# Kernel optimization log

Measured on AMD Instinct MI355X. Metric: run time of the kernel, lower is better.

The kernel has to match this reference:

```python
import jax, jax.numpy as jnp
import numpy as np

H = 512  # hidden_size


def _gru_layer(x, Wi, bi, Wh, bh):
    # x: (B, S, D). Precompute input-to-hidden part for all steps.
    B, S, _ = x.shape
    ip = jnp.einsum('bsd,gd->sbg', x, Wi) + bi  # (S, B, 3H)
    h0 = jnp.zeros((B, H), dtype=x.dtype)

    def step(h, ip_t):
        hp = h @ Wh.T + bh                      # (B, 3H)
        r = jax.nn.sigmoid(ip_t[:, :H] + hp[:, :H])
        z = jax.nn.sigmoid(ip_t[:, H:2*H] + hp[:, H:2*H])
        n = jnp.tanh(ip_t[:, 2*H:] + r * hp[:, 2*H:])
        hy = (1.0 - z) * n + z * h
        return hy, hy

    h_last, ys = jax.lax.scan(step, h0, ip)     # ys: (S, B, H)
    return jnp.transpose(ys, (1, 0, 2)), h_last  # (B, S, H), (B, H)


def setup_inputs() -> dict:
    key = jax.random.key(0)
    ks = jax.random.split(key, 9)
    s = 1.0 / np.sqrt(H)
    d = {
        'x': jax.random.normal(ks[0], (32, 2048, 512), dtype=jnp.float32),
        'Wi0': jax.random.uniform(ks[1], (3*H, 512), jnp.float32, -s, s),
        'bi0': jax.random.uniform(ks[2], (3*H,), jnp.float32, -s, s),
        'Wh0': jax.random.uniform(ks[3], (3*H, H), jnp.float32, -s, s),
        'bh0': jax.random.uniform(ks[4], (3*H,), jnp.float32, -s, s),
        'Wi1': jax.random.uniform(ks[5], (3*H, H), jnp.float32, -s, s),
        'bi1': jax.random.uniform(ks[6], (3*H,), jnp.float32, -s, s),
        'Wh1': jax.random.uniform(ks[7], (3*H, H), jnp.float32, -s, s),
        'bh1': jax.random.uniform(ks[8], (3*H,), jnp.float32, -s, s),
    }
    return d


def reference(x, Wi0, bi0, Wh0, bh0, Wi1, bi1, Wh1, bh1):
    y0, _ = _gru_layer(x, Wi0, bi0, Wh0, bh0)
    y1, h1 = _gru_layer(y0, Wi1, bi1, Wh1, bh1)
    return y1, h1  # outputs (B,S,H), last hidden (B,H)
```

## Files before the change

### kernel.cpp

```cpp
#include <hip/hip_runtime.h>
#include <hip/hip_bf16.h>


typedef __bf16    bf16x8 __attribute__((ext_vector_type(8)));
typedef __bf16    bf16x4 __attribute__((ext_vector_type(4)));
typedef float     f32x4  __attribute__((ext_vector_type(4)));
typedef _Float16  f16x2  __attribute__((ext_vector_type(2)));
typedef _Float16  f16x8  __attribute__((ext_vector_type(8)));

#define S_LEN 2048
#define BATCH 32
#define HID   512
#define G3    1536
#define MROWS (BATCH * S_LEN)
#define NWG   16
#define NFL   64

__device__ inline float sigmoid_f(float x) { return 1.f / (1.f + __expf(-x)); }
__device__ inline float tanh_f(float x) {
  float e = __expf(2.f * x);
  return 1.f - 2.f / (e + 1.f);
}

template <typename IPT>
__device__ inline void store_ip(IPT* p, float v) {
  if constexpr (sizeof(IPT) == 4) *p = v;
  else *p = __builtin_bit_cast(unsigned short, (__bf16)v);
}
template <typename IPT>
__device__ inline float4 load_ip4(const IPT* p) {
  if constexpr (sizeof(IPT) == 4) {
    return *(const float4*)p;
  } else {
    ushort4 u = *(const ushort4*)p;
    float4 r;
    r.x = __uint_as_float((unsigned)u.x << 16);
    r.y = __uint_as_float((unsigned)u.y << 16);
    r.z = __uint_as_float((unsigned)u.z << 16);
    r.w = __uint_as_float((unsigned)u.w << 16);
    return r;
  }
}

__global__ void prep_wib(const float* __restrict__ W, __bf16* __restrict__ o) {
  int i = blockIdx.x * 256 + threadIdx.x;
  o[i] = (__bf16)W[i];
}

__global__ void prep_bfrag(const float* __restrict__ W, unsigned int* __restrict__ out) {
  int idx = blockIdx.x * 256 + threadIdx.x;
  int p    = idx / 24576;
  int r    = idx % 24576;
  int mh   = r / 12288;
  int r2   = r % 12288;
  int frag = r2 / 256;
  int lq   = r2 % 256;
  int l    = lq >> 2, d = lq & 3;
  int g    = frag >> 4, ks = frag & 15;
  int row  = g * 512 + p * 32 + mh * 16 + (l & 15);
  int k    = ks * 32 + (l >> 4) * 8 + 2 * d;
  f16x2 pk = { (_Float16)W[(size_t)row * HID + k],
               (_Float16)W[(size_t)row * HID + k + 1] };
  out[idx] = __builtin_bit_cast(unsigned int, pk);
}

template <typename IPT>
__global__ __launch_bounds__(256) void gemm_ip(
    const float* __restrict__ A, const __bf16* __restrict__ Bw,
    const float* __restrict__ bias, IPT* __restrict__ C) {
  constexpr int K = 512;
  __shared__ __align__(16) __bf16 As[64][72];
  __shared__ __align__(16) __bf16 Bs[64][72];
  const int tid  = threadIdx.x;
  const int bm   = blockIdx.y, bn = blockIdx.x;
  const int lane = tid & 63,  wave = tid >> 6;
  const int wr   = wave >> 1, wc   = wave & 1;
  f32x4 acc[2][2] = {};
  const int r = tid >> 2, q = tid & 3;
  const float*  Arow = A  + (size_t)(bm * 64 + r) * K;
  const __bf16* Brow = Bw + (size_t)(bn * 64 + r) * K;

  for (int k0 = 0; k0 < K; k0 += 64) {
    const float4* as = (const float4*)(Arow + k0);
    #pragma unroll
    for (int i = 0; i < 4; ++i) {
      float4 v = as[q + 4 * i];
      bf16x4 pkt = { (__bf16)v.x, (__bf16)v.y, (__bf16)v.z, (__bf16)v.w };
      *(bf16x4*)&As[r][4 * (q + 4 * i)] = pkt;
    }
    const uint4* bs = (const uint4*)(Brow + k0);
    uint4* bd = (uint4*)&Bs[r][0];
    bd[q]     = bs[q];
    bd[q + 4] = bs[q + 4];
    __syncthreads();

    #pragma unroll
    for (int kk = 0; kk < 64; kk += 32) {
      const int kb = kk + 8 * (lane >> 4);
      bf16x8 a0 = *(const bf16x8*)&As[wr * 32 +      (lane & 15)][kb];
      bf16x8 a1 = *(const bf16x8*)&As[wr * 32 + 16 + (lane & 15)][kb];
      bf16x8 b0 = *(const bf16x8*)&Bs[wc * 32 +      (lane & 15)][kb];
      bf16x8 b1 = *(const bf16x8*)&Bs[wc * 32 + 16 + (lane & 15)][kb];
      acc[0][0] = __builtin_amdgcn_mfma_f32_16x16x32_bf16(a0, b0, acc[0][0], 0, 0, 0);
      acc[0][1] = __builtin_amdgcn_mfma_f32_16x16x32_bf16(a0, b1, acc[0][1], 0, 0, 0);
      acc[1][0] = __builtin_amdgcn_mfma_f32_16x16x32_bf16(a1, b0, acc[1][0], 0, 0, 0);
      acc[1][1] = __builtin_amdgcn_mfma_f32_16x16x32_bf16(a1, b1, acc[1][1], 0, 0, 0);
    }
    __syncthreads();
  }

  const int row0 = bm * 64 + wr * 32 + (lane >> 4) * 4;
  const int col0 = bn * 64 + wc * 32 + (lane & 15);
  #pragma unroll
  for (int fm = 0; fm < 2; ++fm)
    #pragma unroll
    for (int fn = 0; fn < 2; ++fn) {
      int n = col0 + fn * 16;
      float bv = bias[n];
      #pragma unroll
      for (int reg = 0; reg < 4; ++reg) {
        size_t off = (size_t)(row0 + fm * 16 + reg) * G3 + n;
        store_ip<IPT>(C + off, acc[fm][fn][reg] + bv);
      }
    }
}

template <typename IPT>
__global__ __launch_bounds__(256, 1) void gru_fused(
    const IPT* __restrict__ ip0,
    const uint4* __restrict__ bfWh0,
    const float* __restrict__ bh0,
    const uint4* __restrict__ bfWh1,
    const uint4* __restrict__ bfWi1,
    const float* __restrict__ bi1,
    const float* __restrict__ bh1,
    float* __restrict__ y1,
    float* __restrict__ hlast,
    unsigned long long* __restrict__ h1buf,
    unsigned long long* __restrict__ y0h,
    unsigned int* __restrict__ fl0,
    unsigned int* __restrict__ fl1) {
  __shared__ __align__(16) uint4 wiB[6144];
  const int bid = blockIdx.x, tid = threadIdx.x;
  const int lane = tid & 63, wave = tid >> 6;
  const int set = wave & 1, mh = wave >> 1;
  const int jj = lane & 15, hi = lane >> 4;
  const int bb = set * 16 + jj;
  const int bbyte = bb * 1024 + hi * 16;
  const int fidx = (lane & 15) * 4 + set + 2 * ((lane >> 4) & 1);

  if (bid < NWG) {
    const int p = bid;
    const int cc0 = p * 32 + mh * 16 + hi * 4;
    uint4 wf[48];
    {
      const uint4* bsrc = bfWh0 + ((size_t)(p * 2 + mh) * 48) * 64 + lane;
      #pragma unroll
      for (int i = 0; i < 48; ++i) wf[i] = bsrc[i * 64];
      #pragma unroll
      for (int i = 0; i < 48; ++i)
        asm volatile("" : "+v"(wf[i].x), "+v"(wf[i].y), "+v"(wf[i].z), "+v"(wf[i].w));
    }
    const float4 bhr4 = *(const float4*)(bh0 + cc0);
    const float4 bhz4 = *(const float4*)(bh0 + 512 + cc0);
    const float4 bhn4 = *(const float4*)(bh0 + 1024 + cc0);
    float hfq[4] = {0.f, 0.f, 0.f, 0.f};

    for (int t = 0; t < S_LEN; ++t) {
      const IPT* bp = ip0 + ((size_t)bb * S_LEN + t) * G3 + cc0;
      float4 ipr = load_ip4<IPT>(bp);
      float4 ipz = load_ip4<IPT>(bp + 512);
      float4 ipn = load_ip4<IPT>(bp + 1024);
      __builtin_amdgcn_sched_barrier(0);

      f32x4 a0 = {}, a1 = {}, a2 = {};
      if (t > 0) {
        const unsigned int* f = fl0 + (size_t)(t - 1) * NFL;
        while (true) {
          unsigned v = __hip_atomic_load(f + fidx, __ATOMIC_RELAXED,
                                         __HIP_MEMORY_SCOPE_AGENT);
          if (__all(v != 0)) break;
          __builtin_amdgcn_s_sleep(1);
        }
        __builtin_amdgcn_sched_barrier(0);

        const char* hb = (const char*)y0h + (size_t)(t - 1) * 32768 + bbyte;
        uint4 bf[16];
        #pragma unroll
        for (int ks = 0; ks < 16; ++ks)
          asm volatile("global_load_dwordx4 %0, %1, off offset:%2 sc0 sc1"
                       : "=v"(bf[ks]) : "v"(hb), "i"(ks * 64) : "memory");
        asm volatile("s_waitcnt vmcnt(0)" ::: "memory");
        __builtin_amdgcn_sched_barrier(0);

        #pragma unroll
        for (int ks = 0; ks < 16; ++ks) {
          f16x8 hv = __builtin_bit_cast(f16x8, bf[ks]);
          a0 = __builtin_amdgcn_mfma_f32_16x16x32_f16(__builtin_bit_cast(f16x8, wf[ks]),      hv, a0, 0, 0, 0);
          a1 = __builtin_amdgcn_mfma_f32_16x16x32_f16(__builtin_bit_cast(f16x8, wf[16 + ks]), hv, a1, 0, 0, 0);
          a2 = __builtin_amdgcn_mfma_f32_16x16x32_f16(__builtin_bit_cast(f16x8, wf[32 + ks]), hv, a2, 0, 0, 0);
        }
      }

      unsigned short hx[4];
      #pragma unroll
      for (int q = 0; q < 4; ++q) {
        float rr = sigmoid_f(a0[q] + (&bhr4.x)[q] + (&ipr.x)[q]);
        float zz = sigmoid_f(a1[q] + (&bhz4.x)[q] + (&ipz.x)[q]);
        float nn = tanh_f((&ipn.x)[q] + rr * (a2[q] + (&bhn4.x)[q]));
        float hy = (1.f - zz) * nn + zz * hfq[q];
        hfq[q] = hy;
        hx[q] = __builtin_bit_cast(unsigned short, (_Float16)hy);
      }
      const unsigned long long hw =
          (unsigned long long)hx[0] | ((unsigned long long)hx[1] << 16) |
          ((unsigned long long)hx[2] << 32) | ((unsigned long long)hx[3] << 48);
      __hip_atomic_store(y0h + (size_t)t * 4096 + (size_t)bb * 128 + (cc0 >> 2), hw,
                         __ATOMIC_RELAXED, __HIP_MEMORY_SCOPE_AGENT);
      asm volatile("s_waitcnt vmcnt(0)" ::: "memory");
      if (lane == 0)
        __hip_atomic_store(fl0 + (size_t)t * NFL + p * 4 + wave, 1u,
                           __ATOMIC_RELAXED, __HIP_MEMORY_SCOPE_AGENT);
    }
  } else {
    const int p = bid - NWG;
    const int cc0 = p * 32 + mh * 16 + hi * 4;
    uint4 wf[48];
    {
      const uint4* bsrc = bfWh1 + ((size_t)(p * 2 + mh) * 48) * 64 + lane;
      #pragma unroll
      for (int i = 0; i < 48; ++i) wf[i] = bsrc[i * 64];
      #pragma unroll
      for (int i = 0; i < 48; ++i)
        asm volatile("" : "+v"(wf[i].x), "+v"(wf[i].y), "+v"(wf[i].z), "+v"(wf[i].w));
    }
    {
      const uint4* src = bfWi1 + (size_t)p * 6144;
      for (int i = tid; i < 6144; i += 256) wiB[i] = src[i];
    }
    const float4 bir4 = *(const float4*)(bi1 + cc0);
    const float4 biz4 = *(const float4*)(bi1 + 512 + cc0);
    const float4 bin4 = *(const float4*)(bi1 + 1024 + cc0);
    const float4 bhr4 = *(const float4*)(bh1 + cc0);
    const float4 bhz4 = *(const float4*)(bh1 + 512 + cc0);
    const float4 bhn4 = *(const float4*)(bh1 + 1024 + cc0);
    float hfq[4] = {0.f, 0.f, 0.f, 0.f};
    const int wb = mh * 3072 + lane;
    __syncthreads();

    f32x4 i0 = {}, i1 = {}, i2 = {};
    {
      const unsigned int* f = fl0;
      while (true) {
        unsigned v = __hip_atomic_load(f + fidx, __ATOMIC_RELAXED,
                                       __HIP_MEMORY_SCOPE_AGENT);
        if (__all(v != 0)) break;
        __builtin_amdgcn_s_sleep(16);
      }
      __builtin_amdgcn_sched_barrier(0);
      uint4 ay[16];
      const char* yb = (const char*)y0h + bbyte;
      #pragma unroll
      for (int ks = 0; ks < 16; ++ks)
        asm volatile("global_load_dwordx4 %0, %1, off offset:%2 sc0 sc1"
                     : "=v"(ay[ks]) : "v"(yb), "i"(ks * 64) : "memory");
      asm volatile("s_waitcnt vmcnt(0)" ::: "memory");
      __builtin_amdgcn_sched_barrier(0);
      #pragma unroll
      for (int ks = 0; ks < 16; ++ks) {
        f16x8 yv = __builtin_bit_cast(f16x8, ay[ks]);
        i0 = __builtin_amdgcn_mfma_f32_16x16x32_f16(__builtin_bit_cast(f16x8, wiB[wb + ks * 64]),        yv, i0, 0, 0, 0);
        i1 = __builtin_amdgcn_mfma_f32_16x16x32_f16(__builtin_bit_cast(f16x8, wiB[wb + (16 + ks) * 64]), yv, i1, 0, 0, 0);
        i2 = __builtin_amdgcn_mfma_f32_16x16x32_f16(__builtin_bit_cast(f16x8, wiB[wb + (32 + ks) * 64]), yv, i2, 0, 0, 0);
      }
    }

    for (int t = 0; t < S_LEN; ++t) {
      if (t > 0) {
        const unsigned int* f = fl1 + (size_t)(t - 1) * NFL;
        while (true) {
          unsigned v = __hip_atomic_load(f + fidx, __ATOMIC_RELAXED,
                                         __HIP_MEMORY_SCOPE_AGENT);
          if (__all(v != 0)) break;
          __builtin_amdgcn_s_sleep(16);
        }
      }
      __builtin_amdgcn_sched_barrier(0);

      uint4 ah[16];
      {
        const char* hb = (const char*)h1buf + (t & 1) * 32768 + bbyte;
        #pragma unroll
        for (int ks = 0; ks < 16; ++ks)
          asm volatile("global_load_dwordx4 %0, %1, off offset:%2 sc0 sc1"
                       : "=v"(ah[ks]) : "v"(hb), "i"(ks * 64) : "memory");
        asm volatile("s_waitcnt vmcnt(0)" ::: "memory");
      }
      __builtin_amdgcn_sched_barrier(0);

      f32x4 c0 = {}, c1 = {}, c2 = {};
      #pragma unroll
      for (int ks = 0; ks < 16; ++ks) {
        f16x8 hv = __builtin_bit_cast(f16x8, ah[ks]);
        c0 = __builtin_amdgcn_mfma_f32_16x16x32_f16(__builtin_bit_cast(f16x8, wf[ks]),      hv, c0, 0, 0, 0);
        c1 = __builtin_amdgcn_mfma_f32_16x16x32_f16(__builtin_bit_cast(f16x8, wf[16 + ks]), hv, c1, 0, 0, 0);
        c2 = __builtin_amdgcn_mfma_f32_16x16x32_f16(__builtin_bit_cast(f16x8, wf[32 + ks]), hv, c2, 0, 0, 0);
      }

      float hyv[4];
      unsigned short hx[4];
      #pragma unroll
      for (int q = 0; q < 4; ++q) {
        float rr = sigmoid_f(i0[q] + c0[q] + (&bir4.x)[q] + (&bhr4.x)[q]);
        float zz = sigmoid_f(i1[q] + c1[q] + (&biz4.x)[q] + (&bhz4.x)[q]);
        float nn = tanh_f((i2[q] + (&bin4.x)[q]) + rr * (c2[q] + (&bhn4.x)[q]));
        float hy = (1.f - zz) * nn + zz * hfq[q];
        hfq[q] = hy;
        hyv[q] = hy;
        hx[q] = __builtin_bit_cast(unsigned short, (_Float16)hy);
      }
      const unsigned long long hw =
          (unsigned long long)hx[0] | ((unsigned long long)hx[1] << 16) |
          ((unsigned long long)hx[2] << 32) | ((unsigned long long)hx[3] << 48);
      __hip_atomic_store(h1buf + ((size_t)((t + 1) & 1)) * 4096 + (size_t)bb * 128 + (cc0 >> 2),
                         hw, __ATOMIC_RELAXED, __HIP_MEMORY_SCOPE_AGENT);
      asm volatile("s_waitcnt vmcnt(0)" ::: "memory");
      if (lane == 0)
        __hip_atomic_store(fl1 + (size_t)t * NFL + p * 4 + wave, 1u,
                           __ATOMIC_RELAXED, __HIP_MEMORY_SCOPE_AGENT);

      float4 yo = { hyv[0], hyv[1], hyv[2], hyv[3] };
      *(float4*)(y1 + ((size_t)bb * S_LEN + t) * HID + cc0) = yo;
      if (t == S_LEN - 1)
        *(float4*)(hlast + (size_t)bb * HID + cc0) = yo;

      if (t + 1 < S_LEN) {
        const unsigned int* f = fl0 + (size_t)(t + 1) * NFL;
        while (true) {
          unsigned v = __hip_atomic_load(f + fidx, __ATOMIC_RELAXED,
                                         __HIP_MEMORY_SCOPE_AGENT);
          if (__all(v != 0)) break;
          __builtin_amdgcn_s_sleep(16);
        }
        __builtin_amdgcn_sched_barrier(0);
        uint4 ay[16];
        const char* yb = (const char*)y0h + (size_t)(t + 1) * 32768 + bbyte;
        #pragma unroll
        for (int ks = 0; ks < 16; ++ks)
          asm volatile("global_load_dwordx4 %0, %1, off offset:%2 sc0 sc1"
                       : "=v"(ay[ks]) : "v"(yb), "i"(ks * 64) : "memory");
        asm volatile("s_waitcnt vmcnt(0)" ::: "memory");
        __builtin_amdgcn_sched_barrier(0);
        i0 = {}; i1 = {}; i2 = {};
        #pragma unroll
        for (int ks = 0; ks < 16; ++ks) {
          f16x8 yv = __builtin_bit_cast(f16x8, ay[ks]);
          i0 = __builtin_amdgcn_mfma_f32_16x16x32_f16(__builtin_bit_cast(f16x8, wiB[wb + ks * 64]),        yv, i0, 0, 0, 0);
          i1 = __builtin_amdgcn_mfma_f32_16x16x32_f16(__builtin_bit_cast(f16x8, wiB[wb + (16 + ks) * 64]), yv, i1, 0, 0, 0);
          i2 = __builtin_amdgcn_mfma_f32_16x16x32_f16(__builtin_bit_cast(f16x8, wiB[wb + (32 + ks) * 64]), yv, i2, 0, 0, 0);
        }
      }
    }
  }
}

#define BFWH0_OFF 0ull
#define BFWH1_OFF 1572864ull
#define BFWI1_OFF 3145728ull
#define WI0_OFF   4718592ull
#define H1_OFF    6291456ull
#define FL0_OFF   6356992ull
#define FL1_OFF   6881280ull
#define Y0H_OFF   7405568ull
#define IP_OFF    74514432ull

template <typename IPT>
static void run_all(const float* x,
                    const float* Wi0, const float* bi0, const float* Wh0, const float* bh0,
                    const float* Wi1, const float* bi1, const float* Wh1, const float* bh1,
                    float* out, char* ws, hipStream_t stream) {
  unsigned int* bfWh0 = (unsigned int*)(ws + BFWH0_OFF);
  unsigned int* bfWh1 = (unsigned int*)(ws + BFWH1_OFF);
  unsigned int* bfWi1 = (unsigned int*)(ws + BFWI1_OFF);
  __bf16* wi0b = (__bf16*)(ws + WI0_OFF);
  unsigned long long* h1buf = (unsigned long long*)(ws + H1_OFF);
  unsigned int* fl0 = (unsigned int*)(ws + FL0_OFF);
  unsigned int* fl1 = (unsigned int*)(ws + FL1_OFF);
  unsigned long long* y0h = (unsigned long long*)(ws + Y0H_OFF);
  IPT* ip = (IPT*)(ws + IP_OFF);
  float* y1    = out;
  float* hlast = out + (size_t)MROWS * HID;

  hipMemsetAsync(ws + H1_OFF, 0, 65536ull + 524288ull + 524288ull, stream);

  prep_bfrag<<<dim3(1536), dim3(256), 0, stream>>>(Wh0, bfWh0);
  prep_bfrag<<<dim3(1536), dim3(256), 0, stream>>>(Wh1, bfWh1);
  prep_bfrag<<<dim3(1536), dim3(256), 0, stream>>>(Wi1, bfWi1);
  prep_wib<<<dim3(3072), dim3(256), 0, stream>>>(Wi0, wi0b);

  gemm_ip<IPT><<<dim3(24, 1024), dim3(256), 0, stream>>>(x, wi0b, bi0, ip);
  gru_fused<IPT><<<dim3(2 * NWG), dim3(256), 0, stream>>>(
      ip, (const uint4*)bfWh0, bh0, (const uint4*)bfWh1, (const uint4*)bfWi1,
      bi1, bh1, y1, hlast, h1buf, y0h, fl0, fl1);
}

extern "C" void kernel_launch(void* const* d_in, const int* in_sizes, int n_in,
                              void* d_out, int out_size, void* d_ws, size_t ws_size,
                              hipStream_t stream) {
  const float* x   = (const float*)d_in[0];
  const float* Wi0 = (const float*)d_in[1];
  const float* bi0 = (const float*)d_in[2];
  const float* Wh0 = (const float*)d_in[3];
  const float* bh0 = (const float*)d_in[4];
  const float* Wi1 = (const float*)d_in[5];
  const float* bi1 = (const float*)d_in[6];
  const float* Wh1 = (const float*)d_in[7];
  const float* bh1 = (const float*)d_in[8];
  float* out = (float*)d_out;
  char*  ws  = (char*)d_ws;

  const size_t need_f32 = IP_OFF + (size_t)MROWS * G3 * 4;
  if (ws_size >= need_f32) {
    run_all<float>(x, Wi0, bi0, Wh0, bh0, Wi1, bi1, Wh1, bh1, out, ws, stream);
  } else {
    run_all<unsigned short>(x, Wi0, bi0, Wh0, bh0, Wi1, bi1, Wh1, bh1, out, ws, stream);
  }
}
```

Baseline: 11.45 ms.

## Merge layer-1 input projection into recurrent step with combined flag wait

Layer-1 input projection for step t previously ran as its own wait-load-MFMA phase after step t-1's output. It now runs inside step t: a single spin loop polls the layer-0 and layer-1 readiness flags (half the lanes each), both operand sets are loaded together, and the input and recurrent MFMAs are interleaved. Sleep in the poll drops from 16 to 1. This shortens the serial critical path per step and overlaps the two matmuls, but moves the input projection onto the dependent chain and spins more often.

```diff
diff --git a/kernel.cpp b/kernel.cpp
--- a/kernel.cpp
+++ b/kernel.cpp
@@ -248,48 +248,33 @@
     const int wb = mh * 3072 + lane;
     __syncthreads();
 
-    f32x4 i0 = {}, i1 = {}, i2 = {};
-    {
-      const unsigned int* f = fl0;
-      while (true) {
-        unsigned v = __hip_atomic_load(f + fidx, __ATOMIC_RELAXED,
-                                       __HIP_MEMORY_SCOPE_AGENT);
-        if (__all(v != 0)) break;
-        __builtin_amdgcn_s_sleep(16);
+    for (int t = 0; t < S_LEN; ++t) {
+      {
+        const unsigned int* f0 = fl0 + (size_t)t * NFL;
+        const unsigned int* f1 = fl1 + (size_t)(t - 1) * NFL;
+        while (true) {
+          unsigned v;
+          if (lane < 32)
+            v = __hip_atomic_load(f0 + fidx, __ATOMIC_RELAXED,
+                                  __HIP_MEMORY_SCOPE_AGENT);
+          else
+            v = (t > 0) ? __hip_atomic_load(f1 + fidx, __ATOMIC_RELAXED,
+                                            __HIP_MEMORY_SCOPE_AGENT)
+                        : 1u;
+          if (__all(v != 0)) break;
+          __builtin_amdgcn_s_sleep(1);
+        }
       }
       __builtin_amdgcn_sched_barrier(0);
-      uint4 ay[16];
-      const char* yb = (const char*)y0h + bbyte;
-      #pragma unroll
-      for (int ks = 0; ks < 16; ++ks)
-        asm volatile("global_load_dwordx4 %0, %1, off offset:%2 sc0 sc1"
-                     : "=v"(ay[ks]) : "v"(yb), "i"(ks * 64) : "memory");
-      asm volatile("s_waitcnt vmcnt(0)" ::: "memory");
-      __builtin_amdgcn_sched_barrier(0);
-      #pragma unroll
-      for (int ks = 0; ks < 16; ++ks) {
-        f16x8 yv = __builtin_bit_cast(f16x8, ay[ks]);
-        i0 = __builtin_amdgcn_mfma_f32_16x16x32_f16(__builtin_bit_cast(f16x8, wiB[wb + ks * 64]),        yv, i0, 0, 0, 0);
-        i1 = __builtin_amdgcn_mfma_f32_16x16x32_f16(__builtin_bit_cast(f16x8, wiB[wb + (16 + ks) * 64]), yv, i1, 0, 0, 0);
-        i2 = __builtin_amdgcn_mfma_f32_16x16x32_f16(__builtin_bit_cast(f16x8, wiB[wb + (32 + ks) * 64]), yv, i2, 0, 0, 0);
-      }
-    }
-
-    for (int t = 0; t < S_LEN; ++t) {
-      if (t > 0) {
-        const unsigned int* f = fl1 + (size_t)(t - 1) * NFL;
-        while (true) {
-          unsigned v = __hip_atomic_load(f + fidx, __ATOMIC_RELAXED,
-                                         __HIP_MEMORY_SCOPE_AGENT);
-          if (__all(v != 0)) break;
-          __builtin_amdgcn_s_sleep(16);
-        }
-      }
-      __builtin_amdgcn_sched_barrier(0);
-
-      uint4 ah[16];
+
+      uint4 ay[16], ah[16];
       {
+        const char* yb = (const char*)y0h + (size_t)t * 32768 + bbyte;
         const char* hb = (const char*)h1buf + (t & 1) * 32768 + bbyte;
+        #pragma unroll
+        for (int ks = 0; ks < 16; ++ks)
+          asm volatile("global_load_dwordx4 %0, %1, off offset:%2 sc0 sc1"
+                       : "=v"(ay[ks]) : "v"(yb), "i"(ks * 64) : "memory");
         #pragma unroll
         for (int ks = 0; ks < 16; ++ks)
           asm volatile("global_load_dwordx4 %0, %1, off offset:%2 sc0 sc1"
@@ -298,12 +283,17 @@
       }
       __builtin_amdgcn_sched_barrier(0);
 
+      f32x4 i0 = {}, i1 = {}, i2 = {};
       f32x4 c0 = {}, c1 = {}, c2 = {};
       #pragma unroll
       for (int ks = 0; ks < 16; ++ks) {
+        f16x8 yv = __builtin_bit_cast(f16x8, ay[ks]);
         f16x8 hv = __builtin_bit_cast(f16x8, ah[ks]);
+        i0 = __builtin_amdgcn_mfma_f32_16x16x32_f16(__builtin_bit_cast(f16x8, wiB[wb + ks * 64]),        yv, i0, 0, 0, 0);
         c0 = __builtin_amdgcn_mfma_f32_16x16x32_f16(__builtin_bit_cast(f16x8, wf[ks]),      hv, c0, 0, 0, 0);
+        i1 = __builtin_amdgcn_mfma_f32_16x16x32_f16(__builtin_bit_cast(f16x8, wiB[wb + (16 + ks) * 64]), yv, i1, 0, 0, 0);
         c1 = __builtin_amdgcn_mfma_f32_16x16x32_f16(__builtin_bit_cast(f16x8, wf[16 + ks]), hv, c1, 0, 0, 0);
+        i2 = __builtin_amdgcn_mfma_f32_16x16x32_f16(__builtin_bit_cast(f16x8, wiB[wb + (32 + ks) * 64]), yv, i2, 0, 0, 0);
         c2 = __builtin_amdgcn_mfma_f32_16x16x32_f16(__builtin_bit_cast(f16x8, wf[32 + ks]), hv, c2, 0, 0, 0);
       }
 
@@ -333,33 +323,6 @@
       *(float4*)(y1 + ((size_t)bb * S_LEN + t) * HID + cc0) = yo;
       if (t == S_LEN - 1)
         *(float4*)(hlast + (size_t)bb * HID + cc0) = yo;
-
-      if (t + 1 < S_LEN) {
-        const unsigned int* f = fl0 + (size_t)(t + 1) * NFL;
-        while (true) {
-          unsigned v = __hip_atomic_load(f + fidx, __ATOMIC_RELAXED,
-                                         __HIP_MEMORY_SCOPE_AGENT);
-          if (__all(v != 0)) break;
-          __builtin_amdgcn_s_sleep(16);
-        }
-        __builtin_amdgcn_sched_barrier(0);
-        uint4 ay[16];
-        const char* yb = (const char*)y0h + (size_t)(t + 1) * 32768 + bbyte;
-        #pragma unroll
-        for (int ks = 0; ks < 16; ++ks)
-          asm volatile("global_load_dwordx4 %0, %1, off offset:%2 sc0 sc1"
-                       : "=v"(ay[ks]) : "v"(yb), "i"(ks * 64) : "memory");
-        asm volatile("s_waitcnt vmcnt(0)" ::: "memory");
-        __builtin_amdgcn_sched_barrier(0);
-        i0 = {}; i1 = {}; i2 = {};
-        #pragma unroll
-        for (int ks = 0; ks < 16; ++ks) {
-          f16x8 yv = __builtin_bit_cast(f16x8, ay[ks]);
-          i0 = __builtin_amdgcn_mfma_f32_16x16x32_f16(__builtin_bit_cast(f16x8, wiB[wb + ks * 64]),        yv, i0, 0, 0, 0);
-          i1 = __builtin_amdgcn_mfma_f32_16x16x32_f16(__builtin_bit_cast(f16x8, wiB[wb + (16 + ks) * 64]), yv, i1, 0, 0, 0);
-          i2 = __builtin_amdgcn_mfma_f32_16x16x32_f16(__builtin_bit_cast(f16x8, wiB[wb + (32 + ks) * 64]), yv, i2, 0, 0, 0);
-        }
-      }
     }
   }
 }
```

New measurement: 12.54 ms. +9.5%, slower.
